# Optimization experiments

Measured on AMD Instinct MI355X. Metric: run time of the kernel, lower is better.

The kernel has to match this reference:

```python
import jax, jax.numpy as jnp
import numpy as np

H = 1024   # hidden_size == memory_size
NH = 4     # num_attention_heads
HD = H // NH
M = 8192   # total memory items
B, S = 4, 2048
EPS = 1e-5


def _ln(x, g, b):
    mu = jnp.mean(x, -1, keepdims=True)
    var = jnp.mean((x - mu) ** 2, -1, keepdims=True)
    return (x - mu) / jnp.sqrt(var + EPS) * g + b


def setup_inputs() -> dict:
    key = jax.random.key(0)
    ks = jax.random.split(key, 16)
    s = 0.02
    return {
        "query_hidden": jax.random.normal(ks[0], (B, S, H), jnp.float32),
        "mem_keys": jax.random.normal(ks[1], (M, H), jnp.float32),
        "importance": jax.random.uniform(ks[2], (M,), jnp.float32),
        "recency": jax.random.uniform(ks[3], (M,), jnp.float32),
        "access_count": jax.random.uniform(ks[4], (M,), jnp.float32),
        "Wq": s * jax.random.normal(ks[5], (H, H), jnp.float32),
        "bq": jnp.zeros((H,), jnp.float32),
        "in_w": s * jax.random.normal(ks[6], (3 * H, H), jnp.float32),
        "in_b": jnp.zeros((3 * H,), jnp.float32),
        "out_w": s * jax.random.normal(ks[7], (H, H), jnp.float32),
        "out_b": jnp.zeros((H,), jnp.float32),
        "gate_w": s * jax.random.normal(ks[8], (H, 2 * H), jnp.float32),
        "gate_b": jnp.zeros((H,), jnp.float32),
        "int_w1": s * jax.random.normal(ks[9], (2 * H, 2 * H), jnp.float32),
        "int_b1": jnp.zeros((2 * H,), jnp.float32),
        "int_ln_g": jnp.ones((2 * H,), jnp.float32),
        "int_ln_b": jnp.zeros((2 * H,), jnp.float32),
        "int_w2": s * jax.random.normal(ks[10], (H, 2 * H), jnp.float32),
        "int_b2": jnp.zeros((H,), jnp.float32),
        "ln1_g": jnp.ones((H,), jnp.float32),
        "ln1_b": jnp.zeros((H,), jnp.float32),
        "ln2_g": jnp.ones((H,), jnp.float32),
        "ln2_b": jnp.zeros((H,), jnp.float32),
        "sel_params": jnp.ones((3,), jnp.float32) / 3.0,
        "top_k": 2048,
    }


def reference(query_hidden, mem_keys, importance, recency, access_count,
              Wq, bq, in_w, in_b, out_w, out_b, gate_w, gate_b,
              int_w1, int_b1, int_ln_g, int_ln_b, int_w2, int_b2,
              ln1_g, ln1_b, ln2_g, ln2_b, sel_params, top_k):
    b, s, _ = query_hidden.shape
    # HTPS selection: softmax-weighted mix of importance / recency / frequency
    w = jax.nn.softmax(sel_params)
    freq = access_count / jnp.max(access_count)
    sel = w[0] * importance + w[1] * recency + w[2] * freq
    _, idx = jax.lax.top_k(sel, top_k)
    mem = mem_keys[idx]                      # [K, H]
    mem_n = _ln(mem, ln1_g, ln1_b)           # layer_norm1 on memory

    q = query_hidden @ Wq.T + bq             # query_proj  [B,S,H]
    wq, wk, wv = in_w[:H], in_w[H:2 * H], in_w[2 * H:]
    bqi, bki, bvi = in_b[:H], in_b[H:2 * H], in_b[2 * H:]
    # Batched MHA: the per-position loop is equivalent to all S queries at once
    Q = (q @ wq.T + bqi).reshape(b, s, NH, HD)
    K = (mem_n @ wk.T + bki).reshape(top_k, NH, HD)   # shared across batch
    V = (mem_n @ wv.T + bvi).reshape(top_k, NH, HD)
    scores = jnp.einsum('bshd,khd->bhsk', Q, K) / jnp.sqrt(jnp.float32(HD))
    attn = jax.nn.softmax(scores, axis=-1)
    ctx = jnp.einsum('bhsk,khd->bshd', attn, V).reshape(b, s, H)
    attn_out = ctx @ out_w.T + out_b

    cat = jnp.concatenate([query_hidden, attn_out], axis=-1)   # [B,S,2H]
    gate = jax.nn.sigmoid(cat @ gate_w.T + gate_b)
    h1 = _ln(cat @ int_w1.T + int_b1, int_ln_g, int_ln_b)
    integ = jax.nn.gelu(h1, approximate=False) @ int_w2.T + int_b2
    return _ln(query_hidden + gate * integ, ln2_g, ln2_b)
```

## Files before the change

kernel.cpp:

```cpp
#include <hip/hip_runtime.h>

#define HDIM 1024
#define MMEM 8192
#define TOPK 2048
#define NROWS 8192
#define LNEPS 1e-5f

typedef unsigned short ushort_t;
typedef __bf16 bf16x8 __attribute__((ext_vector_type(8)));
typedef float f32x4 __attribute__((ext_vector_type(4)));
typedef __attribute__((address_space(1))) const void GVoid;
typedef __attribute__((address_space(3))) void LVoid;

__device__ __forceinline__ ushort_t f2bf(float f) {
    union { float f; unsigned u; } c; c.f = f;
    unsigned r = c.u + 0x7fffu + ((c.u >> 16) & 1u);
    return (ushort_t)(r >> 16);
}
__device__ __forceinline__ float bf2f(ushort_t u) {
    union { unsigned u; float f; } c; c.u = ((unsigned)u) << 16; return c.f;
}
__device__ __forceinline__ float blk_red(float v, int op, float* red) {
    #pragma unroll
    for (int o = 32; o; o >>= 1) {
        float u = __shfl_down(v, o);
        v = op ? fmaxf(v, u) : v + u;
    }
    if ((threadIdx.x & 63) == 0) red[threadIdx.x >> 6] = v;
    __syncthreads();
    float r = op ? fmaxf(fmaxf(red[0], red[1]), fmaxf(red[2], red[3]))
                 : (red[0] + red[1]) + (red[2] + red[3]);
    __syncthreads();
    return r;
}

__global__ __launch_bounds__(256) void sel_prep(const float* __restrict__ sp,
        const float* __restrict__ imp, const float* __restrict__ rec,
        const float* __restrict__ ac, float* __restrict__ sel) {
    __shared__ float red[4];
    float p0 = sp[0], p1 = sp[1], p2 = sp[2];
    float mx = fmaxf(p0, fmaxf(p1, p2));
    float e0 = expf(p0 - mx), e1 = expf(p1 - mx), e2 = expf(p2 - mx);
    float inv = 1.f / (e0 + e1 + e2);
    float w0 = e0 * inv, w1 = e1 * inv, w2 = e2 * inv;
    float m = -1e30f;
    for (int i = threadIdx.x; i < MMEM; i += 256) m = fmaxf(m, ac[i]);
    m = blk_red(m, 1, red);
    float rinv = 1.f / m;
    for (int i = threadIdx.x; i < MMEM; i += 256)
        sel[i] = w0 * imp[i] + w1 * rec[i] + w2 * (ac[i] * rinv);
}

__global__ __launch_bounds__(256) void topk_rank(const float* __restrict__ sel,
                                                 int* __restrict__ idx) {
    __shared__ float s[MMEM];
    __shared__ int pc[256];
    for (int t = threadIdx.x; t < MMEM / 4; t += 256)
        reinterpret_cast<float4*>(s)[t] = reinterpret_cast<const float4*>(sel)[t];
    __syncthreads();
    const int li = threadIdx.x & 31;
    const int jc = threadIdx.x >> 5;
    const int i  = blockIdx.x * 32 + li;
    const float si = s[i];
    int cnt = 0;
    const float4* sv = reinterpret_cast<const float4*>(s) + jc * 256;
    #pragma unroll 4
    for (int t = 0; t < 256; ++t) {
        float4 v = sv[t];
        int j0 = jc * 1024 + t * 4;
        cnt += (v.x > si) || (v.x == si && (j0 + 0) < i);
        cnt += (v.y > si) || (v.y == si && (j0 + 1) < i);
        cnt += (v.z > si) || (v.z == si && (j0 + 2) < i);
        cnt += (v.w > si) || (v.w == si && (j0 + 3) < i);
    }
    pc[threadIdx.x] = cnt;
    __syncthreads();
    if (threadIdx.x < 32) {
        int r = 0;
        #pragma unroll
        for (int c = 0; c < 8; ++c) r += pc[c * 32 + threadIdx.x];
        if (r < TOPK) idx[r] = blockIdx.x * 32 + threadIdx.x;
    }
}

__global__ __launch_bounds__(256) void gather_ln(const float* __restrict__ mem_keys,
        const int* __restrict__ idx, const float* __restrict__ g,
        const float* __restrict__ b, ushort_t* __restrict__ out) {
    __shared__ float red[4];
    int src = idx[blockIdx.x] & (MMEM - 1);
    const float* x = mem_keys + (size_t)src * HDIM;
    float4 v = reinterpret_cast<const float4*>(x)[threadIdx.x];
    float s = v.x + v.y + v.z + v.w;
    float ss = v.x*v.x + v.y*v.y + v.z*v.z + v.w*v.w;
    s  = blk_red(s, 0, red);
    ss = blk_red(ss, 0, red);
    float mu = s * (1.f / HDIM);
    float var = ss * (1.f / HDIM) - mu * mu;
    float rstd = rsqrtf(var + LNEPS);
    int c = threadIdx.x * 4;
    ushort4 o;
    o.x = f2bf((v.x - mu) * rstd * g[c+0] + b[c+0]);
    o.y = f2bf((v.y - mu) * rstd * g[c+1] + b[c+1]);
    o.z = f2bf((v.z - mu) * rstd * g[c+2] + b[c+2]);
    o.w = f2bf((v.w - mu) * rstd * g[c+3] + b[c+3]);
    *reinterpret_cast<ushort4*>(out + (size_t)blockIdx.x * HDIM + c) = o;
}

__global__ __launch_bounds__(256) void cvt_bf16(const float* __restrict__ in,
                                                ushort_t* __restrict__ out) {
    size_t i = ((size_t)blockIdx.x * 256 + threadIdx.x) * 4;
    float4 v = *reinterpret_cast<const float4*>(in + i);
    ushort4 o = { f2bf(v.x), f2bf(v.y), f2bf(v.z), f2bf(v.w) };
    *reinterpret_cast<ushort4*>(out + i) = o;
}

__global__ __launch_bounds__(256) void cvt_all(const float* __restrict__ in_w,
        const float* __restrict__ gate_w, const float* __restrict__ int_w1,
        const float* __restrict__ int_w2,
        ushort_t* __restrict__ inw_bf, ushort_t* __restrict__ gw3,
        ushort_t* __restrict__ intw2_bf) {
    const int b = blockIdx.x;
    const float* src; ushort_t* dst; int rel;
    if      (b < 3072) { src = in_w;   dst = inw_bf;        rel = b; }
    else if (b < 5120) { src = gate_w; dst = gw3;           rel = b - 3072; }
    else if (b < 9216) { src = int_w1; dst = gw3 + 2097152; rel = b - 5120; }
    else               { src = int_w2; dst = intw2_bf;      rel = b - 9216; }
    size_t i = ((size_t)rel * 256 + threadIdx.x) * 4;
    float4 v = *reinterpret_cast<const float4*>(src + i);
    ushort4 o = { f2bf(v.x), f2bf(v.y), f2bf(v.z), f2bf(v.w) };
    *reinterpret_cast<ushort4*>(dst + i) = o;
}

__global__ __launch_bounds__(256) void cvt_t_bf16(const float* __restrict__ in,
                                                  ushort_t* __restrict__ out) {
    __shared__ ushort_t t[64][65];
    const int bx = blockIdx.x * 64, by = blockIdx.y * 64;
    const int r = threadIdx.x >> 4, c4 = (threadIdx.x & 15) << 2;
    #pragma unroll
    for (int rr = 0; rr < 64; rr += 16) {
        float4 v = *reinterpret_cast<const float4*>(in + (size_t)(by + r + rr) * 1024 + bx + c4);
        t[r + rr][c4 + 0] = f2bf(v.x);
        t[r + rr][c4 + 1] = f2bf(v.y);
        t[r + rr][c4 + 2] = f2bf(v.z);
        t[r + rr][c4 + 3] = f2bf(v.w);
    }
    __syncthreads();
    #pragma unroll
    for (int rr = 0; rr < 64; rr += 16) {
        const int i = r + rr;
        ushort4 o = { t[c4 + 0][i], t[c4 + 1][i], t[c4 + 2][i], t[c4 + 3][i] };
        *reinterpret_cast<ushort4*>(out + (size_t)(bx + i) * 1024 + by + c4) = o;
    }
}

__global__ __launch_bounds__(256) void bias_fold(const float* __restrict__ wq,
        const float* __restrict__ bq, const float* __restrict__ bqi,
        float* __restrict__ beff) {
    __shared__ float red[4];
    const float4 wv = reinterpret_cast<const float4*>(wq + (size_t)blockIdx.x * 1024)[threadIdx.x];
    const float4 bv = reinterpret_cast<const float4*>(bq)[threadIdx.x];
    float s = wv.x*bv.x + wv.y*bv.y + wv.z*bv.z + wv.w*bv.w;
    s = blk_red(s, 0, red);
    if (threadIdx.x == 0) beff[blockIdx.x] = s + bqi[blockIdx.x];
}

__global__ __launch_bounds__(256) void bias_fold3(const float* __restrict__ gate_w,
        const float* __restrict__ int_w1, const float* __restrict__ gate_b,
        const float* __restrict__ int_b1, const float* __restrict__ out_b,
        float* __restrict__ beff3) {
    __shared__ float red[4];
    const int j = blockIdx.x;
    const float* wrow = (j < 1024 ? gate_w + (size_t)j * 2048
                                  : int_w1 + (size_t)(j - 1024) * 2048) + 1024;
    const float4 wv = reinterpret_cast<const float4*>(wrow)[threadIdx.x];
    const float4 bv = reinterpret_cast<const float4*>(out_b)[threadIdx.x];
    float s = wv.x*bv.x + wv.y*bv.y + wv.z*bv.z + wv.w*bv.w;
    s = blk_red(s, 0, red);
    if (threadIdx.x == 0)
        beff3[j] = s + (j < 1024 ? gate_b[j] : int_b1[j - 1024]);
}

__global__ __launch_bounds__(256) void softmax_rows(ushort_t* __restrict__ sc) {
    const int row = blockIdx.x * 4 + (threadIdx.x >> 6);
    const int l = threadIdx.x & 63;
    uint4* p = reinterpret_cast<uint4*>(sc + (size_t)row * 2048 + l * 32);
    uint4 u[4];
    #pragma unroll
    for (int i = 0; i < 4; ++i) u[i] = p[i];
    float v[32];
    #pragma unroll
    for (int i = 0; i < 4; ++i) {
        unsigned* w = reinterpret_cast<unsigned*>(&u[i]);
        #pragma unroll
        for (int k = 0; k < 4; ++k) {
            union { unsigned u; float f; } lo, hi;
            lo.u = w[k] << 16; hi.u = w[k] & 0xffff0000u;
            v[i*8 + k*2]     = lo.f;
            v[i*8 + k*2 + 1] = hi.f;
        }
    }
    float mx = v[0];
    #pragma unroll
    for (int j = 1; j < 32; ++j) mx = fmaxf(mx, v[j]);
    #pragma unroll
    for (int o = 1; o < 64; o <<= 1) mx = fmaxf(mx, __shfl_xor(mx, o));
    float s = 0.f;
    #pragma unroll
    for (int j = 0; j < 32; ++j) { v[j] = __expf(v[j] - mx); s += v[j]; }
    #pragma unroll
    for (int o = 1; o < 64; o <<= 1) s += __shfl_xor(s, o);
    float inv = 1.f / s;
    #pragma unroll
    for (int i = 0; i < 4; ++i) {
        unsigned* w = reinterpret_cast<unsigned*>(&u[i]);
        #pragma unroll
        for (int k = 0; k < 4; ++k) {
            unsigned lo = f2bf(v[i*8 + k*2] * inv);
            unsigned hi = f2bf(v[i*8 + k*2 + 1] * inv);
            w[k] = lo | (hi << 16);
        }
    }
    #pragma unroll
    for (int i = 0; i < 4; ++i) p[i] = u[i];
}

__global__ __launch_bounds__(256) void ln_gelu(ushort_t* h1,
        const float* __restrict__ g, const float* __restrict__ b) {
    __shared__ float red[4];
    ushort_t* p = h1 + (size_t)blockIdx.x * 2048 + threadIdx.x * 8;
    ushort4 a = reinterpret_cast<const ushort4*>(p)[0];
    ushort4 c = reinterpret_cast<const ushort4*>(p)[1];
    float v[8] = { bf2f(a.x), bf2f(a.y), bf2f(a.z), bf2f(a.w),
                   bf2f(c.x), bf2f(c.y), bf2f(c.z), bf2f(c.w) };
    float s = 0.f, ss = 0.f;
    #pragma unroll
    for (int j = 0; j < 8; ++j) { s += v[j]; ss += v[j]*v[j]; }
    s  = blk_red(s, 0, red);
    ss = blk_red(ss, 0, red);
    float mu = s * (1.f / 2048.f);
    float var = ss * (1.f / 2048.f) - mu * mu;
    float rstd = rsqrtf(var + LNEPS);
    int c0 = threadIdx.x * 8;
    ushort_t o[8];
    #pragma unroll
    for (int j = 0; j < 8; ++j) {
        float xn = (v[j] - mu) * rstd * g[c0 + j] + b[c0 + j];
        float ge = 0.5f * xn * (1.f + erff(xn * 0.70710678118654752f));
        o[j] = f2bf(ge);
    }
    ushort4 o1 = { o[0], o[1], o[2], o[3] };
    ushort4 o2 = { o[4], o[5], o[6], o[7] };
    reinterpret_cast<ushort4*>(p)[0] = o1;
    reinterpret_cast<ushort4*>(p)[1] = o2;
}

__global__ __launch_bounds__(256) void final_ln(const float* __restrict__ x,
        const ushort_t* __restrict__ gate, const ushort_t* __restrict__ integ,
        const float* __restrict__ g, const float* __restrict__ b,
        float* __restrict__ out) {
    __shared__ float red[4];
    size_t base = (size_t)blockIdx.x * HDIM + threadIdx.x * 4;
    float4 xv = *reinterpret_cast<const float4*>(x + base);
    ushort4 gv = *reinterpret_cast<const ushort4*>(gate + base);
    ushort4 iv = *reinterpret_cast<const ushort4*>(integ + base);
    float v[4] = { xv.x + bf2f(gv.x)*bf2f(iv.x), xv.y + bf2f(gv.y)*bf2f(iv.y),
                   xv.z + bf2f(gv.z)*bf2f(iv.z), xv.w + bf2f(gv.w)*bf2f(iv.w) };
    float s = v[0]+v[1]+v[2]+v[3];
    float ss = v[0]*v[0]+v[1]*v[1]+v[2]*v[2]+v[3]*v[3];
    s  = blk_red(s, 0, red);
    ss = blk_red(ss, 0, red);
    float mu = s * (1.f / HDIM);
    float var = ss * (1.f / HDIM) - mu * mu;
    float rstd = rsqrtf(var + LNEPS);
    int c = threadIdx.x * 4;
    float4 o;
    o.x = (v[0] - mu) * rstd * g[c+0] + b[c+0];
    o.y = (v[1] - mu) * rstd * g[c+1] + b[c+1];
    o.z = (v[2] - mu) * rstd * g[c+2] + b[c+2];
    o.w = (v[3] - mu) * rstd * g[c+3] + b[c+3];
    *reinterpret_cast<float4*>(out + base) = o;
}

template<int EPI, int BIAS, int SPLIT>
__global__ __launch_bounds__(256, 2)
void gemm_bt(const ushort_t* __restrict__ A, const ushort_t* __restrict__ B,
             const ushort_t* __restrict__ A2, const ushort_t* __restrict__ B2,
             int lda2, int ldb2,
             const float* __restrict__ bias, void* __restrict__ Cv,
             void* __restrict__ Cv2, const float* __restrict__ bias2,
             int K, int lda, int ldb, int ldc,
             long long sA1, long long sA2s, long long sAz,
             long long sB1, long long sB2s, long long sBz,
             long long sC1, long long sC2s, long long sCz,
             int z2n, int zbase, float scale)
{
    __shared__ __align__(16) ushort_t As[8192];
    __shared__ __align__(16) ushort_t Bs[8192];
    const int zz = blockIdx.z;
    const int zg = zz + zbase;
    const int z1 = zg / z2n, z2 = zg - z1 * z2n;
    A += (size_t)(z1 * sA1 + z2 * sA2s + zz * sAz);
    B += (size_t)(z1 * sB1 + z2 * sB2s + zz * sBz);
    const size_t cOff = (size_t)(z1 * sC1 + z2 * sC2s + zz * sCz);

    const int nwg = gridDim.x * gridDim.y;
    const int wg  = blockIdx.y * gridDim.x + blockIdx.x;
    const int q8  = nwg >> 3, r8 = nwg & 7;
    const int xcd = wg & 7, lo = wg >> 3;
    const int wgid = (xcd < r8 ? xcd * (q8 + 1) : r8 * (q8 + 1) + (xcd - r8) * q8) + lo;
    const int m0 = (wgid / gridDim.x) * 128, n0 = (wgid % gridDim.x) * 128;

    const int tid = threadIdx.x;
    const int w = tid >> 6, l = tid & 63;
    const int wm = w >> 1, wn = w & 1;

    f32x4 acc[4][4] = {};
    const int srow = l >> 3;
    const int scol = ((l & 7) ^ srow) << 3;

    for (int k0 = 0; k0 < K; k0 += 64) {
        const ushort_t* Ab = A; const ushort_t* Bb = B;
        int la = lda, lb = ldb, kk0 = k0;
        if (SPLIT && k0 >= 1024) { Ab = A2; Bb = B2; la = lda2; lb = ldb2; kk0 = k0 - 1024; }
        #pragma unroll
        for (int i = 0; i < 4; ++i) {
            const int c = i * 4 + w;
            const int row = c * 8 + srow;
            const ushort_t* ga = Ab + (size_t)(m0 + row) * la + (kk0 + scol);
            const ushort_t* gb = Bb + (size_t)(n0 + row) * lb + (kk0 + scol);
            __builtin_amdgcn_global_load_lds((GVoid*)ga, (LVoid*)(As + c * 512), 16, 0, 0);
            __builtin_amdgcn_global_load_lds((GVoid*)gb, (LVoid*)(Bs + c * 512), 16, 0, 0);
        }
        __syncthreads();
        #pragma unroll
        for (int kk = 0; kk < 2; ++kk) {
            bf16x8 af[4], bfv[4];
            #pragma unroll
            for (int m = 0; m < 4; ++m) {
                const int row = wm * 64 + m * 16 + (l & 15);
                const int cb = ((kk * 64) + ((l >> 4) * 16)) ^ ((row & 7) << 4);
                af[m] = *reinterpret_cast<const bf16x8*>(
                    reinterpret_cast<const char*>(As) + row * 128 + cb);
            }
            #pragma unroll
            for (int n = 0; n < 4; ++n) {
                const int row = wn * 64 + n * 16 + (l & 15);
                const int cb = ((kk * 64) + ((l >> 4) * 16)) ^ ((row & 7) << 4);
                bfv[n] = *reinterpret_cast<const bf16x8*>(
                    reinterpret_cast<const char*>(Bs) + row * 128 + cb);
            }
            #pragma unroll
            for (int m = 0; m < 4; ++m)
                #pragma unroll
                for (int n = 0; n < 4; ++n)
                    acc[m][n] = __builtin_amdgcn_mfma_f32_16x16x32_bf16(
                        af[m], bfv[n], acc[m][n], 0, 0, 0);
        }
        __syncthreads();
    }

    #pragma unroll
    for (int m = 0; m < 4; ++m) {
        const int grow = m0 + wm * 64 + m * 16 + ((l >> 4) << 2);
        #pragma unroll
        for (int n = 0; n < 4; ++n) {
            const int gcol = n0 + wn * 64 + n * 16 + (l & 15);
            float bc = (BIAS == 1) ? bias[gcol] : 0.f;
            #pragma unroll
            for (int j = 0; j < 4; ++j) {
                if (EPI == 3) {
                    float v = acc[m][n][j];
                    if (gcol < 1024) {
                        v += bias[gcol];
                        v = 1.f / (1.f + __expf(-v));
                        ((ushort_t*)Cv)[(size_t)(grow + j) * ldc + gcol] = f2bf(v);
                    } else {
                        v += bias2[gcol - 1024];
                        ((ushort_t*)Cv2)[(size_t)(grow + j) * 2048 + (gcol - 1024)] = f2bf(v);
                    }
                } else {
                    float v = acc[m][n][j] * scale;
                    if (BIAS == 1) v += bc;
                    if (BIAS == 2) v += bias[grow + j];
                    if (EPI == 2) v = 1.f / (1.f + __expf(-v));
                    const size_t off = cOff + (size_t)(grow + j) * ldc + gcol;
                    if (EPI == 1) ((ushort_t*)Cv)[off] = f2bf(v);
                    else          ((float*)Cv)[off]    = v;
                }
            }
        }
    }
}

extern "C" void kernel_launch(void* const* d_in, const int* in_sizes, int n_in,
                              void* d_out, int out_size, void* d_ws, size_t ws_size,
                              hipStream_t stream) {
    const float* x          = (const float*)d_in[0];
    const float* mem_keys   = (const float*)d_in[1];
    const float* importance = (const float*)d_in[2];
    const float* recency    = (const float*)d_in[3];
    const float* access_cnt = (const float*)d_in[4];
    const float* Wq         = (const float*)d_in[5];
    const float* bq         = (const float*)d_in[6];
    const float* in_w       = (const float*)d_in[7];
    const float* in_b       = (const float*)d_in[8];
    const float* out_w      = (const float*)d_in[9];
    const float* out_b      = (const float*)d_in[10];
    const float* gate_w     = (const float*)d_in[11];
    const float* gate_b     = (const float*)d_in[12];
    const float* int_w1     = (const float*)d_in[13];
    const float* int_b1     = (const float*)d_in[14];
    const float* int_ln_g   = (const float*)d_in[15];
    const float* int_ln_b   = (const float*)d_in[16];
    const float* int_w2     = (const float*)d_in[17];
    const float* int_b2     = (const float*)d_in[18];
    const float* ln1_g      = (const float*)d_in[19];
    const float* ln1_b      = (const float*)d_in[20];
    const float* ln2_g      = (const float*)d_in[21];
    const float* ln2_b      = (const float*)d_in[22];
    const float* sel_params = (const float*)d_in[23];

    char* ws = (char*)d_ws;
    size_t off = 0;
    auto alloc = [&](size_t bytes) -> char* {
        char* p = ws + off;
        off = (off + bytes + 255) & ~(size_t)255;
        return p;
    };

    float*    sel      = (float*)alloc(MMEM * 4);
    int*      idx      = (int*)alloc(TOPK * 4);
    float*    beff     = (float*)alloc(1024 * 4);
    float*    beff3    = (float*)alloc(3072 * 4);
    ushort_t* wqT_bf   = (ushort_t*)alloc((size_t)1048576 * 2);
    ushort_t* outwT_bf = (ushort_t*)alloc((size_t)1048576 * 2);
    ushort_t* weff_bf  = (ushort_t*)alloc((size_t)1048576 * 2);
    ushort_t* inw_bf   = (ushort_t*)alloc((size_t)3145728 * 2);
    ushort_t* gw3      = (ushort_t*)alloc((size_t)6291456 * 2);
    ushort_t* wfold3   = (ushort_t*)alloc((size_t)3145728 * 2);
    ushort_t* intw2_bf = (ushort_t*)alloc((size_t)2097152 * 2);
    ushort_t* mem_n    = (ushort_t*)alloc((size_t)TOPK * HDIM * 2);
    ushort_t* Kbuf     = (ushort_t*)alloc((size_t)TOPK * HDIM * 2);
    ushort_t* Vt       = (ushort_t*)alloc((size_t)HDIM * TOPK * 2);
    ushort_t* xbf      = (ushort_t*)alloc((size_t)NROWS * HDIM * 2);
    ushort_t* qQ       = (ushort_t*)alloc((size_t)NROWS * 2048 * 2);
    ushort_t* Qbuf     = qQ + (size_t)NROWS * HDIM;
    ushort_t* h1       = qQ;
    ushort_t* ctx      = (ushort_t*)alloc((size_t)NROWS * HDIM * 2);
    ushort_t* integ    = ctx;

    int NC = 16;
    while (NC > 1 && off + (size_t)NC * 8388608 > ws_size) NC >>= 1;
    ushort_t* scores = (ushort_t*)alloc((size_t)NC * 8388608);
    ushort_t* gatev  = scores;

    cvt_t_bf16<<<dim3(16,16), 256, 0, stream>>>(Wq, wqT_bf);
    cvt_t_bf16<<<dim3(16,16), 256, 0, stream>>>(out_w, outwT_bf);
    cvt_all<<<11264, 256, 0, stream>>>(in_w, gate_w, int_w1, int_w2,
                                       inw_bf, gw3, intw2_bf);
    cvt_bf16<<<8192, 256, 0, stream>>>(x, xbf);
    bias_fold<<<1024, 256, 0, stream>>>(in_w, bq, in_b, beff);
    bias_fold3<<<3072, 256, 0, stream>>>(gate_w, int_w1, gate_b, int_b1, out_b, beff3);

    gemm_bt<1,0,0><<<dim3(8,8,1), 256, 0, stream>>>(inw_bf, wqT_bf,
        nullptr, nullptr, 0, 0, nullptr, weff_bf, nullptr, nullptr,
        1024, 1024, 1024, 1024, 0,0,0, 0,0,0, 0,0,0, 1, 0, 1.f);
    gemm_bt<1,0,0><<<dim3(8,24,1), 256, 0, stream>>>(gw3 + 1024, outwT_bf,
        nullptr, nullptr, 0, 0, nullptr, wfold3, nullptr, nullptr,
        1024, 2048, 1024, 1024, 0,0,0, 0,0,0, 0,0,0, 1, 0, 1.f);

    sel_prep<<<1, 256, 0, stream>>>(sel_params, importance, recency, access_cnt, sel);
    topk_rank<<<MMEM/32, 256, 0, stream>>>(sel, idx);
    gather_ln<<<TOPK, 256, 0, stream>>>(mem_keys, idx, ln1_g, ln1_b, mem_n);

    gemm_bt<1,1,0><<<dim3(8,64,1), 256, 0, stream>>>(xbf, weff_bf,
        nullptr, nullptr, 0, 0, beff, Qbuf, nullptr, nullptr,
        1024, 1024, 1024, 1024, 0,0,0, 0,0,0, 0,0,0, 1, 0, 1.f);
    gemm_bt<1,1,0><<<dim3(8,16,1), 256, 0, stream>>>(mem_n, inw_bf + 1048576,
        nullptr, nullptr, 0, 0, in_b + 1024, Kbuf, nullptr, nullptr,
        1024, 1024, 1024, 1024, 0,0,0, 0,0,0, 0,0,0, 1, 0, 1.f);
    gemm_bt<1,2,0><<<dim3(16,8,1), 256, 0, stream>>>(inw_bf + 2097152, mem_n,
        nullptr, nullptr, 0, 0, in_b + 2048, Vt, nullptr, nullptr,
        1024, 1024, 1024, 2048, 0,0,0, 0,0,0, 0,0,0, 1, 0, 1.f);

    for (int c0 = 0; c0 < 16; c0 += NC) {
        gemm_bt<1,0,0><<<dim3(16,16,NC), 256, 0, stream>>>(Qbuf, Kbuf,
            nullptr, nullptr, 0, 0, nullptr, scores, nullptr, nullptr,
            256, 1024, 1024, 2048,
            2097152, 256, 0,  0, 256, 0,  0, 0, 4194304, 4, c0, 0.0625f);
        softmax_rows<<<NC * 512, 256, 0, stream>>>(scores);
        gemm_bt<1,0,0><<<dim3(2,16,NC), 256, 0, stream>>>(scores, Vt,
            nullptr, nullptr, 0, 0, nullptr, ctx, nullptr, nullptr,
            2048, 2048, 2048, 1024,
            0, 0, 4194304,  0, 524288, 0,  2097152, 256, 0, 4, c0, 1.f);
    }

    gemm_bt<3,0,1><<<dim3(24,64,1), 256, 0, stream>>>(xbf, gw3,
        ctx, wfold3, 1024, 1024, beff3, gatev, h1, beff3 + 1024,
        2048, 1024, 2048, 1024, 0,0,0, 0,0,0, 0,0,0, 1, 0, 1.f);

    ln_gelu<<<NROWS, 256, 0, stream>>>(h1, int_ln_g, int_ln_b);
    gemm_bt<1,1,0><<<dim3(8,64,1), 256, 0, stream>>>(h1, intw2_bf,
        nullptr, nullptr, 0, 0, int_b2, integ, nullptr, nullptr,
        2048, 2048, 2048, 1024, 0,0,0, 0,0,0, 0,0,0, 1, 0, 1.f);
    final_ln<<<NROWS, 256, 0, stream>>>(x, gatev, integ, ln2_g, ln2_b, (float*)d_out);
}
```

Baseline: 572.5 us.

## Fuse softmax into score GEMM epilogue with deferred row normalization

The score GEMM now applies exp in its epilogue, writes unnormalized bf16 probabilities and accumulates per-row sums via shared and global atomics. The PV GEMM divides by the row sum in its epilogue, so the separate softmax_rows pass over the score matrix is gone. It also merges the selection-prep kernel into topk_rank (each block recomputes the scores) and merges the transpose-convert and bias-fold kernel pairs to cut launches. The max subtraction is dropped, which relies on scores being small enough not to overflow exp, and the atomic row sums add nondeterminism and a memset.

Result: slower. 610.4 us (+6.6%).

```diff
diff --git a/kernel.cpp b/kernel.cpp
--- a/kernel.cpp
+++ b/kernel.cpp
@@ -34,29 +34,23 @@
     return r;
 }
 
-__global__ __launch_bounds__(256) void sel_prep(const float* __restrict__ sp,
+__global__ __launch_bounds__(256) void topk_rank(const float* __restrict__ sp,
         const float* __restrict__ imp, const float* __restrict__ rec,
-        const float* __restrict__ ac, float* __restrict__ sel) {
+        const float* __restrict__ ac, int* __restrict__ idx) {
+    __shared__ float s[MMEM];
+    __shared__ int pc[256];
     __shared__ float red[4];
     float p0 = sp[0], p1 = sp[1], p2 = sp[2];
-    float mx = fmaxf(p0, fmaxf(p1, p2));
-    float e0 = expf(p0 - mx), e1 = expf(p1 - mx), e2 = expf(p2 - mx);
-    float inv = 1.f / (e0 + e1 + e2);
-    float w0 = e0 * inv, w1 = e1 * inv, w2 = e2 * inv;
+    float mx3 = fmaxf(p0, fmaxf(p1, p2));
+    float e0 = __expf(p0 - mx3), e1 = __expf(p1 - mx3), e2 = __expf(p2 - mx3);
+    float inv3 = 1.f / (e0 + e1 + e2);
+    float w0 = e0 * inv3, w1 = e1 * inv3, w2 = e2 * inv3;
     float m = -1e30f;
     for (int i = threadIdx.x; i < MMEM; i += 256) m = fmaxf(m, ac[i]);
     m = blk_red(m, 1, red);
     float rinv = 1.f / m;
     for (int i = threadIdx.x; i < MMEM; i += 256)
-        sel[i] = w0 * imp[i] + w1 * rec[i] + w2 * (ac[i] * rinv);
-}
-
-__global__ __launch_bounds__(256) void topk_rank(const float* __restrict__ sel,
-                                                 int* __restrict__ idx) {
-    __shared__ float s[MMEM];
-    __shared__ int pc[256];
-    for (int t = threadIdx.x; t < MMEM / 4; t += 256)
-        reinterpret_cast<float4*>(s)[t] = reinterpret_cast<const float4*>(sel)[t];
+        s[i] = w0 * imp[i] + w1 * rec[i] + w2 * (ac[i] * rinv);
     __syncthreads();
     const int li = threadIdx.x & 31;
     const int jc = threadIdx.x >> 5;
@@ -131,9 +125,12 @@
     *reinterpret_cast<ushort4*>(dst + i) = o;
 }
 
-__global__ __launch_bounds__(256) void cvt_t_bf16(const float* __restrict__ in,
-                                                  ushort_t* __restrict__ out) {
+__global__ __launch_bounds__(256) void cvt_t2(const float* __restrict__ a,
+        const float* __restrict__ b, ushort_t* __restrict__ oa,
+        ushort_t* __restrict__ ob) {
     __shared__ ushort_t t[64][65];
+    const float* in = blockIdx.z ? b : a;
+    ushort_t* out   = blockIdx.z ? ob : oa;
     const int bx = blockIdx.x * 64, by = blockIdx.y * 64;
     const int r = threadIdx.x >> 4, c4 = (threadIdx.x & 15) << 2;
     #pragma unroll
@@ -153,75 +150,33 @@
     }
 }
 
-__global__ __launch_bounds__(256) void bias_fold(const float* __restrict__ wq,
-        const float* __restrict__ bq, const float* __restrict__ bqi,
-        float* __restrict__ beff) {
+__global__ __launch_bounds__(256) void bias_folds(const float* __restrict__ in_w,
+        const float* __restrict__ bq, const float* __restrict__ in_b,
+        const float* __restrict__ gate_w, const float* __restrict__ int_w1,
+        const float* __restrict__ gate_b, const float* __restrict__ int_b1,
+        const float* __restrict__ out_b, float* __restrict__ beff,
+        float* __restrict__ beff3) {
     __shared__ float red[4];
-    const float4 wv = reinterpret_cast<const float4*>(wq + (size_t)blockIdx.x * 1024)[threadIdx.x];
-    const float4 bv = reinterpret_cast<const float4*>(bq)[threadIdx.x];
+    const int b = blockIdx.x;
+    const float* wrow; const float* vec;
+    if (b < 1024) { wrow = in_w + (size_t)b * 1024; vec = bq; }
+    else {
+        const int j = b - 1024;
+        wrow = (j < 1024 ? gate_w + (size_t)j * 2048
+                         : int_w1 + (size_t)(j - 1024) * 2048) + 1024;
+        vec = out_b;
+    }
+    const float4 wv = reinterpret_cast<const float4*>(wrow)[threadIdx.x];
+    const float4 bv = reinterpret_cast<const float4*>(vec)[threadIdx.x];
     float s = wv.x*bv.x + wv.y*bv.y + wv.z*bv.z + wv.w*bv.w;
     s = blk_red(s, 0, red);
-    if (threadIdx.x == 0) beff[blockIdx.x] = s + bqi[blockIdx.x];
-}
-
-__global__ __launch_bounds__(256) void bias_fold3(const float* __restrict__ gate_w,
-        const float* __restrict__ int_w1, const float* __restrict__ gate_b,
-        const float* __restrict__ int_b1, const float* __restrict__ out_b,
-        float* __restrict__ beff3) {
-    __shared__ float red[4];
-    const int j = blockIdx.x;
-    const float* wrow = (j < 1024 ? gate_w + (size_t)j * 2048
-                                  : int_w1 + (size_t)(j - 1024) * 2048) + 1024;
-    const float4 wv = reinterpret_cast<const float4*>(wrow)[threadIdx.x];
-    const float4 bv = reinterpret_cast<const float4*>(out_b)[threadIdx.x];
-    float s = wv.x*bv.x + wv.y*bv.y + wv.z*bv.z + wv.w*bv.w;
-    s = blk_red(s, 0, red);
-    if (threadIdx.x == 0)
-        beff3[j] = s + (j < 1024 ? gate_b[j] : int_b1[j - 1024]);
-}
-
-__global__ __launch_bounds__(256) void softmax_rows(ushort_t* __restrict__ sc) {
-    const int row = blockIdx.x * 4 + (threadIdx.x >> 6);
-    const int l = threadIdx.x & 63;
-    uint4* p = reinterpret_cast<uint4*>(sc + (size_t)row * 2048 + l * 32);
-    uint4 u[4];
-    #pragma unroll
-    for (int i = 0; i < 4; ++i) u[i] = p[i];
-    float v[32];
-    #pragma unroll
-    for (int i = 0; i < 4; ++i) {
-        unsigned* w = reinterpret_cast<unsigned*>(&u[i]);
-        #pragma unroll
-        for (int k = 0; k < 4; ++k) {
-            union { unsigned u; float f; } lo, hi;
-            lo.u = w[k] << 16; hi.u = w[k] & 0xffff0000u;
-            v[i*8 + k*2]     = lo.f;
-            v[i*8 + k*2 + 1] = hi.f;
-        }
-    }
-    float mx = v[0];
-    #pragma unroll
-    for (int j = 1; j < 32; ++j) mx = fmaxf(mx, v[j]);
-    #pragma unroll
-    for (int o = 1; o < 64; o <<= 1) mx = fmaxf(mx, __shfl_xor(mx, o));
-    float s = 0.f;
-    #pragma unroll
-    for (int j = 0; j < 32; ++j) { v[j] = __expf(v[j] - mx); s += v[j]; }
-    #pragma unroll
-    for (int o = 1; o < 64; o <<= 1) s += __shfl_xor(s, o);
-    float inv = 1.f / s;
-    #pragma unroll
-    for (int i = 0; i < 4; ++i) {
-        unsigned* w = reinterpret_cast<unsigned*>(&u[i]);
-        #pragma unroll
-        for (int k = 0; k < 4; ++k) {
-            unsigned lo = f2bf(v[i*8 + k*2] * inv);
-            unsigned hi = f2bf(v[i*8 + k*2 + 1] * inv);
-            w[k] = lo | (hi << 16);
-        }
-    }
-    #pragma unroll
-    for (int i = 0; i < 4; ++i) p[i] = u[i];
+    if (threadIdx.x == 0) {
+        if (b < 1024) beff[b] = s + in_b[b];
+        else {
+            const int j = b - 1024;
+            beff3[j] = s + (j < 1024 ? gate_b[j] : int_b1[j - 1024]);
+        }
+    }
 }
 
 __global__ __launch_bounds__(256) void ln_gelu(ushort_t* h1,
@@ -288,6 +243,7 @@
              int lda2, int ldb2,
              const float* __restrict__ bias, void* __restrict__ Cv,
              void* __restrict__ Cv2, const float* __restrict__ bias2,
+             float* __restrict__ rowsum,
              int K, int lda, int ldb, int ldc,
              long long sA1, long long sA2s, long long sAz,
              long long sB1, long long sB2s, long long sBz,
@@ -359,9 +315,42 @@
         __syncthreads();
     }
 
+    if (EPI == 4) {
+        float* rs = reinterpret_cast<float*>(As);
+        for (int t = tid; t < 128; t += 256) rs[t] = 0.f;
+        __syncthreads();
+        #pragma unroll
+        for (int m = 0; m < 4; ++m) {
+            const int rl = wm * 64 + m * 16 + ((l >> 4) << 2);
+            float psum[4] = {0.f, 0.f, 0.f, 0.f};
+            #pragma unroll
+            for (int n = 0; n < 4; ++n) {
+                const int gcol = n0 + wn * 64 + n * 16 + (l & 15);
+                #pragma unroll
+                for (int j = 0; j < 4; ++j) {
+                    float e = __expf(acc[m][n][j] * scale);
+                    ((ushort_t*)Cv)[cOff + (size_t)(m0 + rl + j) * ldc + gcol] = f2bf(e);
+                    psum[j] += e;
+                }
+            }
+            #pragma unroll
+            for (int j = 0; j < 4; ++j) atomicAdd(&rs[rl + j], psum[j]);
+        }
+        __syncthreads();
+        for (int t = tid; t < 128; t += 256)
+            atomicAdd(rowsum + (size_t)zg * 2048 + m0 + t, rs[t]);
+        return;
+    }
+
     #pragma unroll
     for (int m = 0; m < 4; ++m) {
         const int grow = m0 + wm * 64 + m * 16 + ((l >> 4) << 2);
+        float rsc[4];
+        if (BIAS == 3) {
+            #pragma unroll
+            for (int j = 0; j < 4; ++j)
+                rsc[j] = 1.f / rowsum[(size_t)zg * 2048 + grow + j];
+        }
         #pragma unroll
         for (int n = 0; n < 4; ++n) {
             const int gcol = n0 + wn * 64 + n * 16 + (l & 15);
@@ -382,7 +371,7 @@
                     float v = acc[m][n][j] * scale;
                     if (BIAS == 1) v += bc;
                     if (BIAS == 2) v += bias[grow + j];
-                    if (EPI == 2) v = 1.f / (1.f + __expf(-v));
+                    if (BIAS == 3) v *= rsc[j];
                     const size_t off = cOff + (size_t)(grow + j) * ldc + gcol;
                     if (EPI == 1) ((ushort_t*)Cv)[off] = f2bf(v);
                     else          ((float*)Cv)[off]    = v;
@@ -428,10 +417,10 @@
         return p;
     };
 
-    float*    sel      = (float*)alloc(MMEM * 4);
     int*      idx      = (int*)alloc(TOPK * 4);
     float*    beff     = (float*)alloc(1024 * 4);
     float*    beff3    = (float*)alloc(3072 * 4);
+    float*    rowsum   = (float*)alloc((size_t)16 * 2048 * 4);
     ushort_t* wqT_bf   = (ushort_t*)alloc((size_t)1048576 * 2);
     ushort_t* outwT_bf = (ushort_t*)alloc((size_t)1048576 * 2);
     ushort_t* weff_bf  = (ushort_t*)alloc((size_t)1048576 * 2);
@@ -454,54 +443,54 @@
     ushort_t* scores = (ushort_t*)alloc((size_t)NC * 8388608);
     ushort_t* gatev  = scores;
 
-    cvt_t_bf16<<<dim3(16,16), 256, 0, stream>>>(Wq, wqT_bf);
-    cvt_t_bf16<<<dim3(16,16), 256, 0, stream>>>(out_w, outwT_bf);
+    cvt_t2<<<dim3(16,16,2), 256, 0, stream>>>(Wq, out_w, wqT_bf, outwT_bf);
     cvt_all<<<11264, 256, 0, stream>>>(in_w, gate_w, int_w1, int_w2,
                                        inw_bf, gw3, intw2_bf);
     cvt_bf16<<<8192, 256, 0, stream>>>(x, xbf);
-    bias_fold<<<1024, 256, 0, stream>>>(in_w, bq, in_b, beff);
-    bias_fold3<<<3072, 256, 0, stream>>>(gate_w, int_w1, gate_b, int_b1, out_b, beff3);
+    bias_folds<<<4096, 256, 0, stream>>>(in_w, bq, in_b, gate_w, int_w1,
+                                         gate_b, int_b1, out_b, beff, beff3);
 
     gemm_bt<1,0,0><<<dim3(8,8,1), 256, 0, stream>>>(inw_bf, wqT_bf,
-        nullptr, nullptr, 0, 0, nullptr, weff_bf, nullptr, nullptr,
+        nullptr, nullptr, 0, 0, nullptr, weff_bf, nullptr, nullptr, nullptr,
         1024, 1024, 1024, 1024, 0,0,0, 0,0,0, 0,0,0, 1, 0, 1.f);
     gemm_bt<1,0,0><<<dim3(8,24,1), 256, 0, stream>>>(gw3 + 1024, outwT_bf,
-        nullptr, nullptr, 0, 0, nullptr, wfold3, nullptr, nullptr,
+        nullptr, nullptr, 0, 0, nullptr, wfold3, nullptr, nullptr, nullptr,
         1024, 2048, 1024, 1024, 0,0,0, 0,0,0, 0,0,0, 1, 0, 1.f);
 
-    sel_prep<<<1, 256, 0, stream>>>(sel_params, importance, recency, access_cnt, sel);
-    topk_rank<<<MMEM/32, 256, 0, stream>>>(sel, idx);
+    topk_rank<<<MMEM/32, 256, 0, stream>>>(sel_params, importance, recency,
+                                           access_cnt, idx);
     gather_ln<<<TOPK, 256, 0, stream>>>(mem_keys, idx, ln1_g, ln1_b, mem_n);
 
     gemm_bt<1,1,0><<<dim3(8,64,1), 256, 0, stream>>>(xbf, weff_bf,
-        nullptr, nullptr, 0, 0, beff, Qbuf, nullptr, nullptr,
+        nullptr, nullptr, 0, 0, beff, Qbuf, nullptr, nullptr, nullptr,
         1024, 1024, 1024, 1024, 0,0,0, 0,0,0, 0,0,0, 1, 0, 1.f);
     gemm_bt<1,1,0><<<dim3(8,16,1), 256, 0, stream>>>(mem_n, inw_bf + 1048576,
-        nullptr, nullptr, 0, 0, in_b + 1024, Kbuf, nullptr, nullptr,
+        nullptr, nullptr, 0, 0, in_b + 1024, Kbuf, nullptr, nullptr, nullptr,
         1024, 1024, 1024, 1024, 0,0,0, 0,0,0, 0,0,0, 1, 0, 1.f);
     gemm_bt<1,2,0><<<dim3(16,8,1), 256, 0, stream>>>(inw_bf + 2097152, mem_n,
-        nullptr, nullptr, 0, 0, in_b + 2048, Vt, nullptr, nullptr,
+        nullptr, nullptr, 0, 0, in_b + 2048, Vt, nullptr, nullptr, nullptr,
         1024, 1024, 1024, 2048, 0,0,0, 0,0,0, 0,0,0, 1, 0, 1.f);
 
+    hipMemsetAsync(rowsum, 0, (size_t)16 * 2048 * 4, stream);
+
     for (int c0 = 0; c0 < 16; c0 += NC) {
-        gemm_bt<1,0,0><<<dim3(16,16,NC), 256, 0, stream>>>(Qbuf, Kbuf,
-            nullptr, nullptr, 0, 0, nullptr, scores, nullptr, nullptr,
+        gemm_bt<4,0,0><<<dim3(16,16,NC), 256, 0, stream>>>(Qbuf, Kbuf,
+            nullptr, nullptr, 0, 0, nullptr, scores, nullptr, nullptr, rowsum,
             256, 1024, 1024, 2048,
             2097152, 256, 0,  0, 256, 0,  0, 0, 4194304, 4, c0, 0.0625f);
-        softmax_rows<<<NC * 512, 256, 0, stream>>>(scores);
-        gemm_bt<1,0,0><<<dim3(2,16,NC), 256, 0, stream>>>(scores, Vt,
-            nullptr, nullptr, 0, 0, nullptr, ctx, nullptr, nullptr,
+        gemm_bt<1,3,0><<<dim3(2,16,NC), 256, 0, stream>>>(scores, Vt,
+            nullptr, nullptr, 0, 0, nullptr, ctx, nullptr, nullptr, rowsum,
             2048, 2048, 2048, 1024,
             0, 0, 4194304,  0, 524288, 0,  2097152, 256, 0, 4, c0, 1.f);
     }
 
     gemm_bt<3,0,1><<<dim3(24,64,1), 256, 0, stream>>>(xbf, gw3,
-        ctx, wfold3, 1024, 1024, beff3, gatev, h1, beff3 + 1024,
+        ctx, wfold3, 1024, 1024, beff3, gatev, h1, beff3 + 1024, nullptr,
         2048, 1024, 2048, 1024, 0,0,0, 0,0,0, 0,0,0, 1, 0, 1.f);
 
     ln_gelu<<<NROWS, 256, 0, stream>>>(h1, int_ln_g, int_ln_b);
     gemm_bt<1,1,0><<<dim3(8,64,1), 256, 0, stream>>>(h1, intw2_bf,
-        nullptr, nullptr, 0, 0, int_b2, integ, nullptr, nullptr,
+        nullptr, nullptr, 0, 0, int_b2, integ, nullptr, nullptr, nullptr,
         2048, 2048, 2048, 1024, 0,0,0, 0,0,0, 0,0,0, 1, 0, 1.f);
     final_ln<<<NROWS, 256, 0, stream>>>(x, gatev, integ, ln2_g, ln2_b, (float*)d_out);
 }
```
